# Kernel tuning notes

Hardware: AMD Instinct MI355X
Metric: run time of the kernel (lower is better)

The kernel has to match this reference:

```python
import jax, jax.numpy as jnp
import numpy as np


def setup_inputs() -> dict:
    key = jax.random.key(0)
    k1, k2 = jax.random.split(key)
    B, S, D = 8, 2048, 128
    x = jax.random.normal(k1, (B, S, D), dtype=jnp.float32)
    y = jax.random.normal(k2, (B, S, D), dtype=jnp.float32)
    return {"x": x, "y": y}


def reference(x, y):
    # m1 = x @ y^T  -> [B, Sx, Sy]; unscaled dot-product attention
    m1 = jnp.einsum('bsd,btd->bst', x, y)
    n1 = jax.nn.softmax(m1, axis=-1)
    o1 = jnp.einsum('bst,btd->bsd', n1, y)   # [B, Sx, D]
    a1 = o1 * x                               # gating multiply

    # symmetric pass: m2 = y @ x^T (== m1 transposed)
    m2 = jnp.einsum('btd,bsd->bts', y, x)
    n2 = jax.nn.softmax(m2, axis=-1)
    o2 = jnp.einsum('bts,bsd->btd', n2, x)   # [B, Sy, D]
    a2 = o2 * y

    return jnp.concatenate([a1, a2], axis=-1)  # [B, S, 2D]
```

## Files before the change

### kernel.cpp

```cpp
#include <hip/hip_runtime.h>
#include <hip/hip_bf16.h>

typedef __attribute__((ext_vector_type(8))) short bf16x8;
typedef __attribute__((ext_vector_type(8))) _Float16 f16x8;
typedef __attribute__((ext_vector_type(4))) float f32x4;
typedef __attribute__((ext_vector_type(4))) unsigned int u32x4;

#define MFMA16B(a, b, c) __builtin_amdgcn_mfma_f32_16x16x32_bf16(a, b, c, 0, 0, 0)
#define MFMA16F(a, b, c) __builtin_amdgcn_mfma_f32_16x16x32_f16(a, b, c, 0, 0, 0)

static constexpr int S = 2048;
static constexpr int D = 128;
static constexpr int QT = 64;
static constexpr int KT = 64;

__device__ inline unsigned short f2b(float f) {
    union { float f; unsigned int u; } v; v.f = f;
    unsigned int u = v.u;
    return (unsigned short)((u + 0x7FFFu + ((u >> 16) & 1u)) >> 16);
}
__device__ inline float b2f(unsigned short h) {
    union { unsigned int u; float f; } v; v.u = ((unsigned int)h) << 16;
    return v.f;
}
__device__ inline unsigned int pack2(float a, float b) {
    return (unsigned int)f2b(a) | ((unsigned int)f2b(b) << 16);
}
__device__ inline unsigned int pkh(float a, float b) {
    union { _Float16 h; unsigned short u; } ua, ub;
    ua.h = (_Float16)a; ub.h = (_Float16)b;
    return (unsigned int)ua.u | ((unsigned int)ub.u << 16);
}

__global__ __launch_bounds__(256) void bimodal_prep(
    const float* __restrict__ X, const float* __restrict__ Y,
    unsigned short* __restrict__ WS)
{
    const int bid = blockIdx.x;
    const int t = bid & 31;
    const int b = (bid >> 5) & 7;
    const int mat = bid >> 8;
    const float* src = mat ? Y : X;
    char* kf = (char*)(WS + (size_t)(mat * 2 + 0) * (8ull * S * D)) + (size_t)(b * 32 + t) * 16384;
    char* vt = (char*)(WS + (size_t)(mat * 2 + 1) * (8ull * S * D)) + (size_t)(b * 32 + t) * 16384;

    __shared__ float ftile[64][129];
    const int tid = threadIdx.x;
    const float* tsrc = src + ((size_t)(b * S + t * 64)) * D;
#pragma unroll
    for (int it = 0; it < 8; ++it) {
        int idx = tid + it * 256;
        int row = idx >> 5, ch = idx & 31;
        float4 v = *(const float4*)(tsrc + (size_t)row * D + ch * 4);
        ftile[row][ch * 4 + 0] = v.x; ftile[row][ch * 4 + 1] = v.y;
        ftile[row][ch * 4 + 2] = v.z; ftile[row][ch * 4 + 3] = v.w;
    }
    __syncthreads();
#pragma unroll
    for (int it = 0; it < 16; ++it) {
        int w = tid + it * 256;
        int row = w >> 6, cp = w & 63;
        unsigned int d = pkh(ftile[row][2 * cp], ftile[row][2 * cp + 1]);
        int byte = row * 256 + cp * 4;
        byte ^= (row & 7) << 4;
        *(unsigned int*)(kf + byte) = d;
    }
#pragma unroll
    for (int it = 0; it < 16; ++it) {
        int w = tid + it * 256;
        int dd = w >> 5, jp = w & 31;
        unsigned int d = pkh(ftile[2 * jp][dd], ftile[2 * jp + 1][dd]);
        int byte = dd * 128 + jp * 4;
        byte ^= (dd & 7) << 4;
        *(unsigned int*)(vt + byte) = d;
    }
}

__global__ __launch_bounds__(256) void bimodal_attn_fp16(
    const float* __restrict__ X, const float* __restrict__ Y,
    const unsigned short* __restrict__ WS, float* __restrict__ Out)
{
    const int orig = blockIdx.x;
    const int wg = (orig & 7) * 64 + (orig >> 3);
    const int qt = wg & 31;
    const int p  = (wg >> 5) & 1;
    const int b  = wg >> 6;

    const float* Q = p ? Y : X;
    const int kvmat = p ? 0 : 1;
    const int ocol = p * D;

    __shared__ unsigned short Ksh[KT * D];
    __shared__ unsigned short Vsh[D * KT];
    __shared__ unsigned int   Psh[4][16 * 36];

    const int tid = threadIdx.x;
    const int wv = tid >> 6;
    const int lane = tid & 63;
    const int c = lane & 15;
    const int g = lane >> 4;
    const int i0 = qt * QT + wv * 16;

    const float* qrow = Q + ((size_t)(b * S + i0 + c)) * D;
    f16x8 qf[4];
#pragma unroll
    for (int kc = 0; kc < 4; ++kc) {
        const float* qp = qrow + kc * 32 + g * 8;
        float4 f0 = *(const float4*)qp;
        float4 f1 = *(const float4*)(qp + 4);
        f16x8 tq;
        tq[0] = (_Float16)f0.x; tq[1] = (_Float16)f0.y; tq[2] = (_Float16)f0.z; tq[3] = (_Float16)f0.w;
        tq[4] = (_Float16)f1.x; tq[5] = (_Float16)f1.y; tq[6] = (_Float16)f1.z; tq[7] = (_Float16)f1.w;
        qf[kc] = tq;
    }

    f32x4 o[8];
#pragma unroll
    for (int nb = 0; nb < 8; ++nb) o[nb] = (f32x4){0.f, 0.f, 0.f, 0.f};
    float m = -1e30f, l = 0.f;

    const char* kfb = (const char*)(WS + (size_t)(kvmat * 2 + 0) * (8ull * S * D)) + (size_t)b * (S * D * 2);
    const char* vtb = (const char*)(WS + (size_t)(kvmat * 2 + 1) * (8ull * S * D)) + (size_t)b * (S * D * 2);
    const int soff = wv * 4096 + lane * 16;

    for (int tt = 0; tt < S / KT; ++tt) {
        __syncthreads();
        {
            const char* kt = kfb + tt * 16384;
            const char* vp = vtb + tt * 16384;
            u32x4 ka[4], va[4];
#pragma unroll
            for (int i = 0; i < 4; ++i) ka[i] = *(const u32x4*)(kt + soff + i * 1024);
#pragma unroll
            for (int i = 0; i < 4; ++i) va[i] = *(const u32x4*)(vp + soff + i * 1024);
#pragma unroll
            for (int i = 0; i < 4; ++i) *(u32x4*)((char*)Ksh + soff + i * 1024) = ka[i];
#pragma unroll
            for (int i = 0; i < 4; ++i) *(u32x4*)((char*)Vsh + soff + i * 1024) = va[i];
        }
        __syncthreads();

        f32x4 sT[4];
        __builtin_amdgcn_s_setprio(1);
#pragma unroll
        for (int nb = 0; nb < 4; ++nb) {
            f32x4 acc = (f32x4){0.f, 0.f, 0.f, 0.f};
#pragma unroll
            for (int kc = 0; kc < 4; ++kc) {
                int byte = (nb * 16 + c) * 256 + kc * 64 + g * 16;
                byte ^= (c & 7) << 4;
                f16x8 kA = *(const f16x8*)((const char*)Ksh + byte);
                acc = MFMA16F(kA, qf[kc], acc);
            }
            sT[nb] = acc;
        }
        __builtin_amdgcn_s_setprio(0);

        float pmax = fmaxf(fmaxf(sT[0][0], sT[0][1]), fmaxf(sT[0][2], sT[0][3]));
#pragma unroll
        for (int nb = 1; nb < 4; ++nb)
            pmax = fmaxf(pmax, fmaxf(fmaxf(sT[nb][0], sT[nb][1]), fmaxf(sT[nb][2], sT[nb][3])));
        pmax = fmaxf(pmax, __shfl_xor(pmax, 16));
        pmax = fmaxf(pmax, __shfl_xor(pmax, 32));
        if (!__all(pmax - m <= 8.f)) {
            float mn = fmaxf(m, pmax);
            float alpha = __expf(m - mn);
            m = mn; l *= alpha;
#pragma unroll
            for (int nb = 0; nb < 8; ++nb) {
                o[nb][0] *= alpha; o[nb][1] *= alpha;
                o[nb][2] *= alpha; o[nb][3] *= alpha;
            }
        }
        float rs = 0.f;
        unsigned int* pr = Psh[wv] + c * 36;
#pragma unroll
        for (int nb = 0; nb < 4; ++nb) {
            float e0 = __expf(sT[nb][0] - m), e1 = __expf(sT[nb][1] - m);
            float e2 = __expf(sT[nb][2] - m), e3 = __expf(sT[nb][3] - m);
            rs += (e0 + e1) + (e2 + e3);
            pr[nb * 8 + 2 * g + 0] = pkh(e0, e1);
            pr[nb * 8 + 2 * g + 1] = pkh(e2, e3);
        }
        rs += __shfl_xor(rs, 16);
        rs += __shfl_xor(rs, 32);
        l += rs;

        __builtin_amdgcn_wave_barrier();

        union { f16x8 v; u32x4 u; } pf0, pf1;
        pf0.u = *(const u32x4*)(Psh[wv] + c * 36 + 0 * 16 + 4 * g);
        pf1.u = *(const u32x4*)(Psh[wv] + c * 36 + 1 * 16 + 4 * g);

        __builtin_amdgcn_s_setprio(1);
#pragma unroll
        for (int nb = 0; nb < 8; ++nb) {
            int byte0 = (nb * 16 + c) * 128 + 0 * 64 + g * 16; byte0 ^= (c & 7) << 4;
            int byte1 = (nb * 16 + c) * 128 + 1 * 64 + g * 16; byte1 ^= (c & 7) << 4;
            f16x8 v0 = *(const f16x8*)((const char*)Vsh + byte0);
            f16x8 v1 = *(const f16x8*)((const char*)Vsh + byte1);
            o[nb] = MFMA16F(v0, pf0.v, o[nb]);
            o[nb] = MFMA16F(v1, pf1.v, o[nb]);
        }
        __builtin_amdgcn_s_setprio(0);
    }

    const float inv = 1.f / l;
    float* outr = Out + ((size_t)(b * S + i0 + c)) * (2 * D) + ocol;
#pragma unroll
    for (int nb = 0; nb < 8; ++nb) {
        int d0 = nb * 16 + 4 * g;
        float4 qv = *(const float4*)(qrow + d0);
        float4 ov;
        ov.x = o[nb][0] * inv * qv.x;
        ov.y = o[nb][1] * inv * qv.y;
        ov.z = o[nb][2] * inv * qv.z;
        ov.w = o[nb][3] * inv * qv.w;
        *(float4*)(outr + d0) = ov;
    }
}

__global__ __launch_bounds__(256) void bimodal_attn_fb(
    const float* __restrict__ X, const float* __restrict__ Y,
    float* __restrict__ Out)
{
    const int bid = blockIdx.x;
    const int qt = bid & 31;
    const int p  = (bid >> 5) & 1;
    const int b  = bid >> 6;

    const float* Q  = p ? Y : X;
    const float* KV = p ? X : Y;
    const int ocol = p * D;

    __shared__ unsigned short Khi[KT * D];
    __shared__ unsigned short Klo[KT * D];
    __shared__ unsigned short Vt[D * KT];
    __shared__ unsigned short Psh[4][16 * 72];

    const int tid = threadIdx.x;
    const int wv = tid >> 6;
    const int lane = tid & 63;
    const int c = lane & 15;
    const int g = lane >> 4;
    const int i0 = qt * QT + wv * 16;

    const float* qbase = Q + ((size_t)(b * S + i0 + c)) * D;
    bf16x8 qhi[4], qlo[4];
#pragma unroll
    for (int kc = 0; kc < 4; ++kc) {
        const float* qp = qbase + kc * 32 + g * 8;
        float4 f0 = *(const float4*)qp;
        float4 f1 = *(const float4*)(qp + 4);
        float fv[8] = {f0.x, f0.y, f0.z, f0.w, f1.x, f1.y, f1.z, f1.w};
        bf16x8 th, tl;
#pragma unroll
        for (int i = 0; i < 8; ++i) {
            unsigned short h = f2b(fv[i]);
            th[i] = (short)h;
            tl[i] = (short)f2b(fv[i] - b2f(h));
        }
        qhi[kc] = th; qlo[kc] = tl;
    }

    f32x4 o[8];
#pragma unroll
    for (int nb = 0; nb < 8; ++nb) { o[nb][0] = 0.f; o[nb][1] = 0.f; o[nb][2] = 0.f; o[nb][3] = 0.f; }
    float m[4], l[4];
#pragma unroll
    for (int r = 0; r < 4; ++r) { m[r] = -1e30f; l[r] = 0.f; }

    const float* kvb = KV + (size_t)b * S * D;
    unsigned short* pbuf = Psh[wv];

    for (int j0 = 0; j0 < S; j0 += KT) {
#pragma unroll
        for (int t = 0; t < 4; ++t) {
            int task = tid + t * 256;
            int jr = task >> 4, sl = task & 15;
            const float* src = kvb + (size_t)(j0 + jr) * D + sl * 8;
            float4 f0 = *(const float4*)src;
            float4 f1 = *(const float4*)(src + 4);
            float fv[8] = {f0.x, f0.y, f0.z, f0.w, f1.x, f1.y, f1.z, f1.w};
            unsigned short hv[8];
            float lv[8];
#pragma unroll
            for (int i = 0; i < 8; ++i) {
                hv[i] = f2b(fv[i]);
                lv[i] = fv[i] - b2f(hv[i]);
            }
            uint4 wh, wl;
            wh.x = (unsigned int)hv[0] | ((unsigned int)hv[1] << 16);
            wh.y = (unsigned int)hv[2] | ((unsigned int)hv[3] << 16);
            wh.z = (unsigned int)hv[4] | ((unsigned int)hv[5] << 16);
            wh.w = (unsigned int)hv[6] | ((unsigned int)hv[7] << 16);
            wl.x = pack2(lv[0], lv[1]); wl.y = pack2(lv[2], lv[3]);
            wl.z = pack2(lv[4], lv[5]); wl.w = pack2(lv[6], lv[7]);
            int byte = jr * 256 + sl * 16;
            byte ^= (jr & 7) << 4;
            *(uint4*)((char*)Khi + byte) = wh;
            *(uint4*)((char*)Klo + byte) = wl;
        }
#pragma unroll
        for (int t = 0; t < 2; ++t) {
            int task = tid + t * 256;
            int jp = task & 31, dc = task >> 5;
            const float* s0 = kvb + (size_t)(j0 + 2 * jp) * D + dc * 8;
            const float* s1 = s0 + D;
            float4 a0 = *(const float4*)s0, a1 = *(const float4*)(s0 + 4);
            float4 b0 = *(const float4*)s1, b1 = *(const float4*)(s1 + 4);
            float av[8] = {a0.x, a0.y, a0.z, a0.w, a1.x, a1.y, a1.z, a1.w};
            float bv[8] = {b0.x, b0.y, b0.z, b0.w, b1.x, b1.y, b1.z, b1.w};
#pragma unroll
            for (int i = 0; i < 8; ++i) {
                int d = dc * 8 + i;
                int byte = d * 128 + jp * 4;
                byte ^= (d & 7) << 4;
                *(unsigned int*)((char*)Vt + byte) = pack2(av[i], bv[i]);
            }
        }
        __syncthreads();

        f32x4 sF[4];
#pragma unroll
        for (int nb = 0; nb < 4; ++nb) {
            f32x4 acc; acc[0] = 0.f; acc[1] = 0.f; acc[2] = 0.f; acc[3] = 0.f;
#pragma unroll
            for (int kc = 0; kc < 4; ++kc) {
                int row = nb * 16 + c;
                int byte = row * 256 + (kc * 32 + g * 8) * 2;
                byte ^= (row & 7) << 4;
                bf16x8 kh = *(const bf16x8*)((char*)Khi + byte);
                bf16x8 kl = *(const bf16x8*)((char*)Klo + byte);
                acc = MFMA16B(qhi[kc], kh, acc);
                acc = MFMA16B(qhi[kc], kl, acc);
                acc = MFMA16B(qlo[kc], kh, acc);
            }
            sF[nb] = acc;
        }

#pragma unroll
        for (int r = 0; r < 4; ++r) {
            float v = fmaxf(fmaxf(sF[0][r], sF[1][r]), fmaxf(sF[2][r], sF[3][r]));
            v = fmaxf(v, __shfl_xor(v, 1));
            v = fmaxf(v, __shfl_xor(v, 2));
            v = fmaxf(v, __shfl_xor(v, 4));
            v = fmaxf(v, __shfl_xor(v, 8));
            float mn = fmaxf(m[r], v);
            float alpha = __expf(m[r] - mn);
            m[r] = mn;
            float rs = 0.f;
#pragma unroll
            for (int nb = 0; nb < 4; ++nb) {
                float pv = __expf(sF[nb][r] - mn);
                sF[nb][r] = pv;
                rs += pv;
            }
            rs += __shfl_xor(rs, 1);
            rs += __shfl_xor(rs, 2);
            rs += __shfl_xor(rs, 4);
            rs += __shfl_xor(rs, 8);
            l[r] = l[r] * alpha + rs;
#pragma unroll
            for (int nb = 0; nb < 8; ++nb) o[nb][r] *= alpha;
        }

#pragma unroll
        for (int nb = 0; nb < 4; ++nb)
#pragma unroll
            for (int r = 0; r < 4; ++r)
                pbuf[(g * 4 + r) * 72 + nb * 16 + c] = f2b(sF[nb][r]);

        bf16x8 pa[2];
#pragma unroll
        for (int kc = 0; kc < 2; ++kc)
            pa[kc] = *(const bf16x8*)(pbuf + c * 72 + kc * 32 + g * 8);

#pragma unroll
        for (int nb = 0; nb < 8; ++nb) {
#pragma unroll
            for (int kc = 0; kc < 2; ++kc) {
                int d = nb * 16 + c;
                int byte = d * 128 + (kc * 32 + g * 8) * 2;
                byte ^= (d & 7) << 4;
                bf16x8 vf = *(const bf16x8*)((char*)Vt + byte);
                o[nb] = MFMA16B(pa[kc], vf, o[nb]);
            }
        }
        __syncthreads();
    }

    float* outb = Out + ((size_t)(b * S + i0)) * (2 * D) + ocol;
    const float* qg = Q + (size_t)(b * S + i0) * D;
#pragma unroll
    for (int r = 0; r < 4; ++r) {
        int row = g * 4 + r;
        float inv = 1.f / l[r];
#pragma unroll
        for (int nb = 0; nb < 8; ++nb) {
            int col = nb * 16 + c;
            float qv = qg[(size_t)row * D + col];
            outb[(size_t)row * (2 * D) + col] = o[nb][r] * inv * qv;
        }
    }
}

extern "C" void kernel_launch(void* const* d_in, const int* in_sizes, int n_in,
                              void* d_out, int out_size, void* d_ws, size_t ws_size,
                              hipStream_t stream) {
    const float* x = (const float*)d_in[0];
    const float* y = (const float*)d_in[1];
    float* out = (float*)d_out;
    const int B = 8;
    dim3 grid(B * 2 * (S / QT));
    dim3 block(256);
    const size_t need = 4ull * 8 * S * D * 2;
    if (ws_size >= need) {
        hipLaunchKernelGGL(bimodal_prep, grid, block, 0, stream, x, y, (unsigned short*)d_ws);
        hipLaunchKernelGGL(bimodal_attn_fp16, grid, block, 0, stream, x, y,
                           (const unsigned short*)d_ws, out);
    } else {
        hipLaunchKernelGGL(bimodal_attn_fb, grid, block, 0, stream, x, y, out);
    }
}
```

Measured before the change: 76.99 us.

## Process two query sub-tiles per wave and prefetch next K/V tile into registers

Each wave now handles 32 query rows (two 16-row sub-tiles), so every K and V fragment read from LDS feeds two MFMAs. The grid is halved to 256 blocks with launch bounds of one block per SIMD group and a new XCD-aware block mapping. The next K/V tile is loaded from global memory into registers before the current tile's compute and written to LDS afterwards, overlapping the global load latency with compute. In exchange, register pressure doubles, and with 256 blocks on 256 CUs there is only one wave per SIMD, which limits latency hiding.

```diff
diff --git a/kernel.cpp b/kernel.cpp
--- a/kernel.cpp
+++ b/kernel.cpp
@@ -11,8 +11,8 @@
 
 static constexpr int S = 2048;
 static constexpr int D = 128;
-static constexpr int QT = 64;
 static constexpr int KT = 64;
+static constexpr int NT = S / KT;
 
 __device__ inline unsigned short f2b(float f) {
     union { float f; unsigned int u; } v; v.f = f;
@@ -76,15 +76,49 @@
     }
 }
 
-__global__ __launch_bounds__(256) void bimodal_attn_fp16(
+__device__ __forceinline__ void softmax_update(
+    f32x4 (&sT)[4], float& m, float& l, f32x4 (&o)[8],
+    unsigned int* pr, int gq)
+{
+    float pmax = fmaxf(fmaxf(sT[0][0], sT[0][1]), fmaxf(sT[0][2], sT[0][3]));
+#pragma unroll
+    for (int nb = 1; nb < 4; ++nb)
+        pmax = fmaxf(pmax, fmaxf(fmaxf(sT[nb][0], sT[nb][1]), fmaxf(sT[nb][2], sT[nb][3])));
+    pmax = fmaxf(pmax, __shfl_xor(pmax, 16));
+    pmax = fmaxf(pmax, __shfl_xor(pmax, 32));
+    if (!__all(pmax - m <= 8.f)) {
+        float mn = fmaxf(m, pmax);
+        float alpha = __expf(m - mn);
+        m = mn; l *= alpha;
+#pragma unroll
+        for (int nb = 0; nb < 8; ++nb) {
+            o[nb][0] *= alpha; o[nb][1] *= alpha;
+            o[nb][2] *= alpha; o[nb][3] *= alpha;
+        }
+    }
+    float rs = 0.f;
+#pragma unroll
+    for (int nb = 0; nb < 4; ++nb) {
+        float e0 = __expf(sT[nb][0] - m), e1 = __expf(sT[nb][1] - m);
+        float e2 = __expf(sT[nb][2] - m), e3 = __expf(sT[nb][3] - m);
+        rs += (e0 + e1) + (e2 + e3);
+        uint2 w; w.x = pkh(e0, e1); w.y = pkh(e2, e3);
+        *(uint2*)(pr + nb * 8 + 2 * gq) = w;
+    }
+    rs += __shfl_xor(rs, 16);
+    rs += __shfl_xor(rs, 32);
+    l += rs;
+}
+
+__global__ __launch_bounds__(256, 1) void bimodal_attn_v2(
     const float* __restrict__ X, const float* __restrict__ Y,
     const unsigned short* __restrict__ WS, float* __restrict__ Out)
 {
-    const int orig = blockIdx.x;
-    const int wg = (orig & 7) * 64 + (orig >> 3);
-    const int qt = wg & 31;
-    const int p  = (wg >> 5) & 1;
-    const int b  = wg >> 6;
+    const int bid = blockIdx.x;
+    const int xcd = bid & 7, slot = bid >> 3;
+    const int g16 = xcd + 8 * (slot >> 4);
+    const int qt  = slot & 15;
+    const int p = g16 & 1, b = g16 >> 1;
 
     const float* Q = p ? Y : X;
     const int kvmat = p ? 0 : 1;
@@ -92,131 +126,143 @@
 
     __shared__ unsigned short Ksh[KT * D];
     __shared__ unsigned short Vsh[D * KT];
-    __shared__ unsigned int   Psh[4][16 * 36];
+    __shared__ unsigned int   Psh[4][2][16 * 36];
 
     const int tid = threadIdx.x;
     const int wv = tid >> 6;
     const int lane = tid & 63;
     const int c = lane & 15;
-    const int g = lane >> 4;
-    const int i0 = qt * QT + wv * 16;
-
-    const float* qrow = Q + ((size_t)(b * S + i0 + c)) * D;
-    f16x8 qf[4];
+    const int gq = lane >> 4;
+    const int i0 = qt * 128 + wv * 32;
+
+    const float* qrow0 = Q + ((size_t)(b * S + i0 + c)) * D;
+    const float* qrow1 = qrow0 + 16 * D;
+    f16x8 qf0[4], qf1[4];
 #pragma unroll
     for (int kc = 0; kc < 4; ++kc) {
-        const float* qp = qrow + kc * 32 + g * 8;
-        float4 f0 = *(const float4*)qp;
-        float4 f1 = *(const float4*)(qp + 4);
-        f16x8 tq;
-        tq[0] = (_Float16)f0.x; tq[1] = (_Float16)f0.y; tq[2] = (_Float16)f0.z; tq[3] = (_Float16)f0.w;
-        tq[4] = (_Float16)f1.x; tq[5] = (_Float16)f1.y; tq[6] = (_Float16)f1.z; tq[7] = (_Float16)f1.w;
-        qf[kc] = tq;
-    }
-
-    f32x4 o[8];
-#pragma unroll
-    for (int nb = 0; nb < 8; ++nb) o[nb] = (f32x4){0.f, 0.f, 0.f, 0.f};
-    float m = -1e30f, l = 0.f;
+        const float* qp0 = qrow0 + kc * 32 + gq * 8;
+        const float* qp1 = qrow1 + kc * 32 + gq * 8;
+        float4 a0 = *(const float4*)qp0, a1 = *(const float4*)(qp0 + 4);
+        float4 b0 = *(const float4*)qp1, b1 = *(const float4*)(qp1 + 4);
+        f16x8 t0, t1;
+        t0[0] = (_Float16)a0.x; t0[1] = (_Float16)a0.y; t0[2] = (_Float16)a0.z; t0[3] = (_Float16)a0.w;
+        t0[4] = (_Float16)a1.x; t0[5] = (_Float16)a1.y; t0[6] = (_Float16)a1.z; t0[7] = (_Float16)a1.w;
+        t1[0] = (_Float16)b0.x; t1[1] = (_Float16)b0.y; t1[2] = (_Float16)b0.z; t1[3] = (_Float16)b0.w;
+        t1[4] = (_Float16)b1.x; t1[5] = (_Float16)b1.y; t1[6] = (_Float16)b1.z; t1[7] = (_Float16)b1.w;
+        qf0[kc] = t0; qf1[kc] = t1;
+    }
+
+    f32x4 o0[8], o1[8];
+#pragma unroll
+    for (int nb = 0; nb < 8; ++nb) { o0[nb] = (f32x4){0.f,0.f,0.f,0.f}; o1[nb] = (f32x4){0.f,0.f,0.f,0.f}; }
+    float m0 = -1e30f, l0 = 0.f, m1 = -1e30f, l1 = 0.f;
 
     const char* kfb = (const char*)(WS + (size_t)(kvmat * 2 + 0) * (8ull * S * D)) + (size_t)b * (S * D * 2);
     const char* vtb = (const char*)(WS + (size_t)(kvmat * 2 + 1) * (8ull * S * D)) + (size_t)b * (S * D * 2);
     const int soff = wv * 4096 + lane * 16;
 
-    for (int tt = 0; tt < S / KT; ++tt) {
-        __syncthreads();
+    u32x4 ka[4], va[4];
+#pragma unroll
+    for (int i = 0; i < 4; ++i) ka[i] = *(const u32x4*)(kfb + soff + i * 1024);
+#pragma unroll
+    for (int i = 0; i < 4; ++i) va[i] = *(const u32x4*)(vtb + soff + i * 1024);
+#pragma unroll
+    for (int i = 0; i < 4; ++i) *(u32x4*)((char*)Ksh + soff + i * 1024) = ka[i];
+#pragma unroll
+    for (int i = 0; i < 4; ++i) *(u32x4*)((char*)Vsh + soff + i * 1024) = va[i];
+    __syncthreads();
+
+    for (int tt = 0; tt < NT; ++tt) {
+        const int tn = (tt + 1 < NT) ? tt + 1 : tt;
         {
-            const char* kt = kfb + tt * 16384;
-            const char* vp = vtb + tt * 16384;
-            u32x4 ka[4], va[4];
+            const char* kt = kfb + tn * 16384;
+            const char* vp = vtb + tn * 16384;
 #pragma unroll
             for (int i = 0; i < 4; ++i) ka[i] = *(const u32x4*)(kt + soff + i * 1024);
 #pragma unroll
             for (int i = 0; i < 4; ++i) va[i] = *(const u32x4*)(vp + soff + i * 1024);
-#pragma unroll
-            for (int i = 0; i < 4; ++i) *(u32x4*)((char*)Ksh + soff + i * 1024) = ka[i];
-#pragma unroll
-            for (int i = 0; i < 4; ++i) *(u32x4*)((char*)Vsh + soff + i * 1024) = va[i];
-        }
-        __syncthreads();
-
-        f32x4 sT[4];
+        }
+
+        f32x4 sT0[4], sT1[4];
         __builtin_amdgcn_s_setprio(1);
 #pragma unroll
         for (int nb = 0; nb < 4; ++nb) {
-            f32x4 acc = (f32x4){0.f, 0.f, 0.f, 0.f};
+            f32x4 a0 = (f32x4){0.f,0.f,0.f,0.f};
+            f32x4 a1 = (f32x4){0.f,0.f,0.f,0.f};
 #pragma unroll
             for (int kc = 0; kc < 4; ++kc) {
-                int byte = (nb * 16 + c) * 256 + kc * 64 + g * 16;
+                int byte = (nb * 16 + c) * 256 + kc * 64 + gq * 16;
                 byte ^= (c & 7) << 4;
                 f16x8 kA = *(const f16x8*)((const char*)Ksh + byte);
-                acc = MFMA16F(kA, qf[kc], acc);
-            }
-            sT[nb] = acc;
+                a0 = MFMA16F(kA, qf0[kc], a0);
+                a1 = MFMA16F(kA, qf1[kc], a1);
+            }
+            sT0[nb] = a0; sT1[nb] = a1;
         }
         __builtin_amdgcn_s_setprio(0);
 
-        float pmax = fmaxf(fmaxf(sT[0][0], sT[0][1]), fmaxf(sT[0][2], sT[0][3]));
-#pragma unroll
-        for (int nb = 1; nb < 4; ++nb)
-            pmax = fmaxf(pmax, fmaxf(fmaxf(sT[nb][0], sT[nb][1]), fmaxf(sT[nb][2], sT[nb][3])));
-        pmax = fmaxf(pmax, __shfl_xor(pmax, 16));
-        pmax = fmaxf(pmax, __shfl_xor(pmax, 32));
-        if (!__all(pmax - m <= 8.f)) {
-            float mn = fmaxf(m, pmax);
-            float alpha = __expf(m - mn);
-            m = mn; l *= alpha;
-#pragma unroll
-            for (int nb = 0; nb < 8; ++nb) {
-                o[nb][0] *= alpha; o[nb][1] *= alpha;
-                o[nb][2] *= alpha; o[nb][3] *= alpha;
-            }
-        }
-        float rs = 0.f;
-        unsigned int* pr = Psh[wv] + c * 36;
-#pragma unroll
-        for (int nb = 0; nb < 4; ++nb) {
-            float e0 = __expf(sT[nb][0] - m), e1 = __expf(sT[nb][1] - m);
-            float e2 = __expf(sT[nb][2] - m), e3 = __expf(sT[nb][3] - m);
-            rs += (e0 + e1) + (e2 + e3);
-            pr[nb * 8 + 2 * g + 0] = pkh(e0, e1);
-            pr[nb * 8 + 2 * g + 1] = pkh(e2, e3);
-        }
-        rs += __shfl_xor(rs, 16);
-        rs += __shfl_xor(rs, 32);
-        l += rs;
+        softmax_update(sT0, m0, l0, o0, &Psh[wv][0][c * 36], gq);
+        softmax_update(sT1, m1, l1, o1, &Psh[wv][1][c * 36], gq);
 
         __builtin_amdgcn_wave_barrier();
 
-        union { f16x8 v; u32x4 u; } pf0, pf1;
-        pf0.u = *(const u32x4*)(Psh[wv] + c * 36 + 0 * 16 + 4 * g);
-        pf1.u = *(const u32x4*)(Psh[wv] + c * 36 + 1 * 16 + 4 * g);
+        union { f16x8 v; u32x4 u; } p00, p01, p10, p11;
+        p00.u = *(const u32x4*)(&Psh[wv][0][c * 36 + 0 * 16 + 4 * gq]);
+        p01.u = *(const u32x4*)(&Psh[wv][0][c * 36 + 1 * 16 + 4 * gq]);
+        p10.u = *(const u32x4*)(&Psh[wv][1][c * 36 + 0 * 16 + 4 * gq]);
+        p11.u = *(const u32x4*)(&Psh[wv][1][c * 36 + 1 * 16 + 4 * gq]);
 
         __builtin_amdgcn_s_setprio(1);
 #pragma unroll
         for (int nb = 0; nb < 8; ++nb) {
-            int byte0 = (nb * 16 + c) * 128 + 0 * 64 + g * 16; byte0 ^= (c & 7) << 4;
-            int byte1 = (nb * 16 + c) * 128 + 1 * 64 + g * 16; byte1 ^= (c & 7) << 4;
+            int byte0 = (nb * 16 + c) * 128 + 0 * 64 + gq * 16; byte0 ^= (c & 7) << 4;
+            int byte1 = (nb * 16 + c) * 128 + 1 * 64 + gq * 16; byte1 ^= (c & 7) << 4;
             f16x8 v0 = *(const f16x8*)((const char*)Vsh + byte0);
             f16x8 v1 = *(const f16x8*)((const char*)Vsh + byte1);
-            o[nb] = MFMA16F(v0, pf0.v, o[nb]);
-            o[nb] = MFMA16F(v1, pf1.v, o[nb]);
+            o0[nb] = MFMA16F(v0, p00.v, o0[nb]);
+            o0[nb] = MFMA16F(v1, p01.v, o0[nb]);
+            o1[nb] = MFMA16F(v0, p10.v, o1[nb]);
+            o1[nb] = MFMA16F(v1, p11.v, o1[nb]);
         }
         __builtin_amdgcn_s_setprio(0);
-    }
-
-    const float inv = 1.f / l;
-    float* outr = Out + ((size_t)(b * S + i0 + c)) * (2 * D) + ocol;
-#pragma unroll
-    for (int nb = 0; nb < 8; ++nb) {
-        int d0 = nb * 16 + 4 * g;
-        float4 qv = *(const float4*)(qrow + d0);
-        float4 ov;
-        ov.x = o[nb][0] * inv * qv.x;
-        ov.y = o[nb][1] * inv * qv.y;
-        ov.z = o[nb][2] * inv * qv.z;
-        ov.w = o[nb][3] * inv * qv.w;
-        *(float4*)(outr + d0) = ov;
+
+        __syncthreads();
+#pragma unroll
+        for (int i = 0; i < 4; ++i) *(u32x4*)((char*)Ksh + soff + i * 1024) = ka[i];
+#pragma unroll
+        for (int i = 0; i < 4; ++i) *(u32x4*)((char*)Vsh + soff + i * 1024) = va[i];
+        __syncthreads();
+    }
+
+    {
+        const float inv = 1.f / l0;
+        float* outr = Out + ((size_t)(b * S + i0 + c)) * (2 * D) + ocol;
+#pragma unroll
+        for (int nb = 0; nb < 8; ++nb) {
+            int d0 = nb * 16 + 4 * gq;
+            float4 qv = *(const float4*)(qrow0 + d0);
+            float4 ov;
+            ov.x = o0[nb][0] * inv * qv.x;
+            ov.y = o0[nb][1] * inv * qv.y;
+            ov.z = o0[nb][2] * inv * qv.z;
+            ov.w = o0[nb][3] * inv * qv.w;
+            *(float4*)(outr + d0) = ov;
+        }
+    }
+    {
+        const float inv = 1.f / l1;
+        float* outr = Out + ((size_t)(b * S + i0 + 16 + c)) * (2 * D) + ocol;
+#pragma unroll
+        for (int nb = 0; nb < 8; ++nb) {
+            int d0 = nb * 16 + 4 * gq;
+            float4 qv = *(const float4*)(qrow1 + d0);
+            float4 ov;
+            ov.x = o1[nb][0] * inv * qv.x;
+            ov.y = o1[nb][1] * inv * qv.y;
+            ov.z = o1[nb][2] * inv * qv.z;
+            ov.w = o1[nb][3] * inv * qv.w;
+            *(float4*)(outr + d0) = ov;
+        }
     }
 }
 
@@ -243,7 +289,7 @@
     const int lane = tid & 63;
     const int c = lane & 15;
     const int g = lane >> 4;
-    const int i0 = qt * QT + wv * 16;
+    const int i0 = qt * 64 + wv * 16;
 
     const float* qbase = Q + ((size_t)(b * S + i0 + c)) * D;
     bf16x8 qhi[4], qlo[4];
@@ -411,15 +457,16 @@
     const float* x = (const float*)d_in[0];
     const float* y = (const float*)d_in[1];
     float* out = (float*)d_out;
-    const int B = 8;
-    dim3 grid(B * 2 * (S / QT));
     dim3 block(256);
     const size_t need = 4ull * 8 * S * D * 2;
     if (ws_size >= need) {
-        hipLaunchKernelGGL(bimodal_prep, grid, block, 0, stream, x, y, (unsigned short*)d_ws);
-        hipLaunchKernelGGL(bimodal_attn_fp16, grid, block, 0, stream, x, y,
+        dim3 pgrid(512);
+        dim3 agrid(256);
+        hipLaunchKernelGGL(bimodal_prep, pgrid, block, 0, stream, x, y, (unsigned short*)d_ws);
+        hipLaunchKernelGGL(bimodal_attn_v2, agrid, block, 0, stream, x, y,
                            (const unsigned short*)d_ws, out);
     } else {
-        hipLaunchKernelGGL(bimodal_attn_fb, grid, block, 0, stream, x, y, out);
-    }
-}
+        dim3 fgrid(512);
+        hipLaunchKernelGGL(bimodal_attn_fb, fgrid, block, 0, stream, x, y, out);
+    }
+}
```

After: 89.17 us. +15.8%, slower.
